# Performance work log

Hardware: AMD Instinct MI355X
Metric: run time of the kernel (lower is better)

The kernel has to match this reference:

```python
import jax, jax.numpy as jnp
import numpy as np

N = 100000
E = 1600000
DIM_IN, DIM_H, DIM_OUT = 48, 48, 48


def gcn_conv(x, edge_index, W, b):
    # PyG GCNConv: add self-loops, symmetric normalization D^-1/2 (A+I) D^-1/2, linear first.
    n = x.shape[0]
    loop = jnp.arange(n, dtype=edge_index.dtype)
    row = jnp.concatenate([edge_index[0], loop])  # sources
    col = jnp.concatenate([edge_index[1], loop])  # targets
    deg = jax.ops.segment_sum(jnp.ones_like(col, dtype=x.dtype), col, num_segments=n)
    dinv = jnp.where(deg > 0, jax.lax.rsqrt(jnp.maximum(deg, 1e-12)), 0.0)
    norm = dinv[row] * dinv[col]  # [E+N]
    h = x @ W  # [N, out]
    msg = h[row] * norm[:, None]  # gather + scale, [E+N, out]
    out = jax.ops.segment_sum(msg, col, num_segments=n)  # scatter-add
    return out + b


def setup_inputs() -> dict:
    key = jax.random.key(0)
    ks = jax.random.split(key, 8)
    x = jax.random.normal(ks[0], (N, DIM_IN), dtype=jnp.float32)
    edge_index = jax.random.randint(ks[1], (2, E), 0, N, dtype=jnp.int64)
    s1 = 1.0 / np.sqrt(DIM_IN)
    s2 = 1.0 / np.sqrt(DIM_H)
    s3 = 1.0 / np.sqrt(DIM_OUT)
    W1 = jax.random.uniform(ks[2], (DIM_IN, DIM_H), jnp.float32, -s1, s1)
    b1 = jnp.zeros((DIM_H,), jnp.float32)
    W2 = jax.random.uniform(ks[3], (DIM_H, DIM_OUT), jnp.float32, -s2, s2)
    b2 = jnp.zeros((DIM_OUT,), jnp.float32)
    Wlin = jax.random.uniform(ks[4], (DIM_OUT, 2), jnp.float32, -s3, s3)
    blin = jax.random.uniform(ks[5], (2,), jnp.float32, -s3, s3)
    return {"x": x, "edge_index": edge_index, "W1": W1, "b1": b1, "W2": W2, "b2": b2, "Wlin": Wlin, "blin": blin}


def reference(x, edge_index, W1, b1, W2, b2, Wlin, blin):
    h = gcn_conv(x, edge_index, W1, b1)
    h = jax.nn.leaky_relu(h, negative_slope=0.01)
    h = gcn_conv(h, edge_index, W2, b2)
    # global_add_pool with all-zero batch ids -> sum over all nodes, [1, DIM_OUT]
    g = jnp.sum(h, axis=0, keepdims=True)
    # dropout is identity in eval mode
    return g @ Wlin + blin  # [1, 2]
```

## Files before the change

kernel.cpp:

```cpp
#include <hip/hip_runtime.h>
#include <hip/hip_bf16.h>
#include <hip/hip_fp8.h>

#define DIM 48
#define HS8 64
#define BKN 128
#define CAP 2816
#define NB1MAX 800
#define NBLK 512
#define GNPB 64
#define GTPN 3

typedef float v2f __attribute__((ext_vector_type(2)));

__device__ inline unsigned pack_fp8x4(float a, float b, float c, float d) {
#if __has_builtin(__builtin_amdgcn_cvt_pk_fp8_f32)
    int w = __builtin_amdgcn_cvt_pk_fp8_f32(a, b, 0, false);
    w = __builtin_amdgcn_cvt_pk_fp8_f32(c, d, w, true);
    return (unsigned)w;
#else
    __hip_fp8_e4m3 qa(a), qb(b), qc(c), qd(d);
    return (unsigned)qa.__x | ((unsigned)qb.__x << 8) |
           ((unsigned)qc.__x << 16) | ((unsigned)qd.__x << 24);
#endif
}

__device__ inline void acc_fp8x4(unsigned w, float* acc) {
#if __has_builtin(__builtin_amdgcn_cvt_pk_f32_fp8)
    v2f lo = __builtin_amdgcn_cvt_pk_f32_fp8((int)w, false);
    v2f hi = __builtin_amdgcn_cvt_pk_f32_fp8((int)w, true);
    acc[0] += lo[0]; acc[1] += lo[1]; acc[2] += hi[0]; acc[3] += hi[1];
#else
    __hip_fp8_e4m3 q0, q1, q2, q3;
    q0.__x = (unsigned char)(w & 0xff);
    q1.__x = (unsigned char)((w >> 8) & 0xff);
    q2.__x = (unsigned char)((w >> 16) & 0xff);
    q3.__x = (unsigned char)(w >> 24);
    acc[0] += (float)q0; acc[1] += (float)q1;
    acc[2] += (float)q2; acc[3] += (float)q3;
#endif
}

__device__ inline void acc_fp8x16(uint4 v, float* acc) {
    acc_fp8x4(v.x, acc + 0);
    acc_fp8x4(v.y, acc + 4);
    acc_fp8x4(v.z, acc + 8);
    acc_fp8x4(v.w, acc + 12);
}

__global__ void k_zero(int* __restrict__ cntc, int* __restrict__ cntr,
                       float* __restrict__ g, int nb1) {
    int i = blockIdx.x * blockDim.x + threadIdx.x;
    if (i < nb1) { cntc[i] = 0; cntr[i] = 0; }
    if (i < 64) g[i] = 0.0f;
}

__global__ void k_part(const int* __restrict__ row, const int* __restrict__ col,
                       int* __restrict__ cntc, int* __restrict__ cntr,
                       unsigned* __restrict__ partc, unsigned* __restrict__ partr,
                       int E, int nb1) {
    __shared__ int hc[NB1MAX], hr[NB1MAX];
    __shared__ int bc_[NB1MAX], br_[NB1MAX];
    int blk = blockIdx.x, t = threadIdx.x;
    for (int i = t; i < nb1; i += blockDim.x) { hc[i] = 0; hr[i] = 0; }
    __syncthreads();
    int chunk = (E + NBLK - 1) / NBLK;
    int lo = blk * chunk, hi = min(lo + chunk, E);
    for (int e = lo + t; e < hi; e += blockDim.x) {
        atomicAdd(&hc[col[e] >> 7], 1);
        atomicAdd(&hr[row[e] >> 7], 1);
    }
    __syncthreads();
    for (int i = t; i < nb1; i += blockDim.x) {
        bc_[i] = hc[i] ? atomicAdd(&cntc[i], hc[i]) : 0;
        br_[i] = hr[i] ? atomicAdd(&cntr[i], hr[i]) : 0;
        hc[i] = 0; hr[i] = 0;
    }
    __syncthreads();
    for (int e = lo + t; e < hi; e += blockDim.x) {
        int c = col[e], r = row[e];
        int bc2 = c >> 7, br2 = r >> 7;
        unsigned pc = (unsigned)(bc_[bc2] + atomicAdd(&hc[bc2], 1));
        if (pc < (unsigned)CAP)
            partc[(size_t)bc2 * CAP + pc] = ((unsigned)(c & 127) << 24) | (unsigned)r;
        unsigned pr = (unsigned)(br_[br2] + atomicAdd(&hr[br2], 1));
        if (pr < (unsigned)CAP)
            partr[(size_t)br2 * CAP + pr] = ((unsigned)(r & 127) << 24) | (unsigned)c;
    }
}

__global__ void k_sortp(const unsigned* __restrict__ partc, const int* __restrict__ cntc,
                        int* __restrict__ nodpk, float* __restrict__ dinv,
                        int* __restrict__ srcs, int N, int nb1) {
    __shared__ int cnt[BKN];
    __shared__ int cur[BKN];
    __shared__ int sc[256];
    __shared__ int outb[CAP];
    int b = blockIdx.x, t = threadIdx.x;
    int nlo = b * BKN;
    int nE = min(cntc[b], CAP);
    const unsigned* pp = partc + (size_t)b * CAP;
    if (t < BKN) cnt[t] = 0;
    __syncthreads();
    for (int e = t; e < nE; e += blockDim.x)
        atomicAdd(&cnt[pp[e] >> 24], 1);
    __syncthreads();
    int v = (t < BKN) ? cnt[t] : 0;
    sc[t] = v;
    __syncthreads();
    for (int off = 1; off < 256; off <<= 1) {
        int u = (t >= off) ? sc[t - off] : 0;
        __syncthreads();
        sc[t] += u;
        __syncthreads();
    }
    int ex = (t == 0) ? 0 : sc[t - 1];
    if (t < BKN && nlo + t < N) {
        nodpk[nlo + t] = ex | (v << 16);
        dinv[nlo + t] = 1.0f / sqrtf((float)(v + 1));
        cur[t] = ex;
    }
    __syncthreads();
    for (int e = t; e < nE; e += blockDim.x) {
        unsigned p = pp[e];
        int s = atomicAdd(&cur[p >> 24], 1);
        outb[s] = (int)(p & 0xffffffu);
    }
    __syncthreads();
    int* sb = srcs + (size_t)b * CAP;
    for (int i2 = t; i2 < nE; i2 += blockDim.x) sb[i2] = outb[i2];
}

__global__ void k_wsum(const unsigned* __restrict__ partr, const int* __restrict__ cntr,
                       const float* __restrict__ dinv, float* __restrict__ wfin,
                       int N, int nb1) {
    __shared__ float ws[BKN];
    int b = blockIdx.x, t = threadIdx.x;
    if (t < BKN) ws[t] = 0.0f;
    __syncthreads();
    int nE = min(cntr[b], CAP);
    const unsigned* pp = partr + (size_t)b * CAP;
    for (int e = t; e < nE; e += blockDim.x) {
        unsigned p = pp[e];
        atomicAdd(&ws[p >> 24], dinv[p & 0xffffffu]);
    }
    __syncthreads();
    int j = b * BKN + t;
    if (t < BKN && j < N) {
        float dj = dinv[j];
        wfin[j] = (ws[t] + dj) * dj;
    }
}

__global__ void k_mm_scale(const float* __restrict__ in, const float* __restrict__ W,
                           const float* __restrict__ dinv,
                           unsigned char* __restrict__ hs8, int n) {
    __shared__ float Ws[DIM * DIM];
    for (int i = threadIdx.x; i < DIM * DIM; i += blockDim.x) Ws[i] = W[i];
    __syncthreads();
    int node = blockIdx.x * blockDim.x + threadIdx.x;
    if (node >= n) return;
    float xr[DIM];
    const float4* xp = (const float4*)(in + (size_t)node * DIM);
    #pragma unroll
    for (int j = 0; j < DIM / 4; ++j) {
        float4 v = xp[j];
        xr[j * 4 + 0] = v.x; xr[j * 4 + 1] = v.y;
        xr[j * 4 + 2] = v.z; xr[j * 4 + 3] = v.w;
    }
    float o[DIM];
    #pragma unroll
    for (int f = 0; f < DIM; ++f) o[f] = 0.0f;
    for (int k = 0; k < DIM; ++k) {
        float xv = xr[k];
        #pragma unroll
        for (int f = 0; f < DIM; ++f) o[f] = fmaf(xv, Ws[k * DIM + f], o[f]);
    }
    float d = dinv[node];
    uint4* hp = (uint4*)(hs8 + (size_t)node * HS8);
    #pragma unroll
    for (int q = 0; q < 3; ++q) {
        uint4 v;
        v.x = pack_fp8x4(o[q*16+ 0]*d, o[q*16+ 1]*d, o[q*16+ 2]*d, o[q*16+ 3]*d);
        v.y = pack_fp8x4(o[q*16+ 4]*d, o[q*16+ 5]*d, o[q*16+ 6]*d, o[q*16+ 7]*d);
        v.z = pack_fp8x4(o[q*16+ 8]*d, o[q*16+ 9]*d, o[q*16+10]*d, o[q*16+11]*d);
        v.w = pack_fp8x4(o[q*16+12]*d, o[q*16+13]*d, o[q*16+14]*d, o[q*16+15]*d);
        hp[q] = v;
    }
}

__global__ __launch_bounds__(GNPB * GTPN) void k_gather1f(
    const unsigned char* __restrict__ hs8,
    const int* __restrict__ nodpk, const int* __restrict__ srcs,
    const float* __restrict__ dinv, const float* __restrict__ wfin,
    const float* __restrict__ bias, float* __restrict__ g, int n) {
    __shared__ float gsum[DIM];
    int t = threadIdx.x;
    if (t < DIM) gsum[t] = 0.0f;
    __syncthreads();
    int local = t / GTPN;
    int c = t - local * GTPN;
    int i = blockIdx.x * GNPB + local;
    bool valid = (i < n);
    float ov[16];
    if (valid) {
        int pk = nodpk[i];
        int start = (i >> 7) * CAP + (pk & 0xffff);
        int end = start + (pk >> 16);
        float d = dinv[i];
        float w = wfin[i];
        const unsigned char* hb = hs8 + (size_t)c * 16;
        float acc[16];
        #pragma unroll
        for (int k = 0; k < 16; ++k) acc[k] = 0.0f;
        uint4 sv = *(const uint4*)(hb + (size_t)i * HS8);
        acc_fp8x16(sv, acc);
        for (int j = start; j < end; ++j) {
            uint4 v = *(const uint4*)(hb + (size_t)srcs[j] * HS8);
            acc_fp8x16(v, acc);
        }
        #pragma unroll
        for (int k = 0; k < 16; ++k) {
            float vv = acc[k] * d + bias[c * 16 + k];
            vv = (vv >= 0.0f) ? vv : 0.01f * vv;
            ov[k] = vv * w;
        }
    }
    if (valid) {
        #pragma unroll
        for (int k = 0; k < 16; ++k) atomicAdd(&gsum[c * 16 + k], ov[k]);
    }
    __syncthreads();
    if (t < DIM) atomicAdd(&g[t], gsum[t]);
}

__global__ void k_final2(const float* __restrict__ g, const float* __restrict__ W2,
                         const float* __restrict__ b2, const float* __restrict__ Wlin,
                         const float* __restrict__ blin, float* __restrict__ out, int n) {
    __shared__ float gp[DIM];
    int t = threadIdx.x;
    if (t < DIM) {
        float s = (float)n * b2[t];
        for (int q = 0; q < DIM; ++q) s += g[q] * W2[q * DIM + t];
        gp[t] = s;
    }
    __syncthreads();
    if (t < 2) {
        float s = blin[t];
        for (int f = 0; f < DIM; ++f) s += gp[f] * Wlin[f * 2 + t];
        out[t] = s;
    }
}

static inline char* alignup(char* p, size_t a) {
    return (char*)(((uintptr_t)p + a - 1) & ~(uintptr_t)(a - 1));
}

extern "C" void kernel_launch(void* const* d_in, const int* in_sizes, int n_in,
                              void* d_out, int out_size, void* d_ws, size_t ws_size,
                              hipStream_t stream) {
    const float* x    = (const float*)d_in[0];
    const int*   ei   = (const int*)d_in[1];
    const float* W1   = (const float*)d_in[2];
    const float* b1   = (const float*)d_in[3];
    const float* W2   = (const float*)d_in[4];
    const float* b2   = (const float*)d_in[5];
    const float* Wlin = (const float*)d_in[6];
    const float* blin = (const float*)d_in[7];
    float* out = (float*)d_out;

    int N = in_sizes[0] / DIM;
    int E = in_sizes[1] / 2;
    const int* row = ei;
    const int* col = ei + E;
    int nb1 = (N + BKN - 1) / BKN;

    char* p = (char*)d_ws;
    int* cntc = (int*)p;                  p = alignup(p + nb1 * 4, 64);
    int* cntr = (int*)p;                  p = alignup(p + nb1 * 4, 64);
    int* nodpk = (int*)p;                 p = alignup(p + (size_t)N * 4, 64);
    float* dinv = (float*)p;              p = alignup(p + (size_t)N * 4, 64);
    float* wfin = (float*)p;              p = alignup(p + (size_t)N * 4, 64);
    float* g = (float*)p;                 p = alignup(p + 64 * 4, 64);
    unsigned* partc = (unsigned*)p;       p = alignup(p + (size_t)nb1 * CAP * 4, 64);
    unsigned* partr = (unsigned*)p;       p = alignup(p + (size_t)nb1 * CAP * 4, 64);
    int* srcs = (int*)p;                  p = alignup(p + (size_t)nb1 * CAP * 4, 64);
    unsigned char* hs8 = (unsigned char*)p;

    int nblk = (N + 255) / 256;
    int gblk = (N + GNPB - 1) / GNPB;

    k_zero<<<(nb1 + 255) / 256, 256, 0, stream>>>(cntc, cntr, g, nb1);
    k_part<<<NBLK, 256, 0, stream>>>(row, col, cntc, cntr, partc, partr, E, nb1);
    k_sortp<<<nb1, 256, 0, stream>>>(partc, cntc, nodpk, dinv, srcs, N, nb1);
    k_wsum<<<nb1, 256, 0, stream>>>(partr, cntr, dinv, wfin, N, nb1);

    k_mm_scale<<<nblk, 256, 0, stream>>>(x, W1, dinv, hs8, N);
    k_gather1f<<<gblk, GNPB * GTPN, 0, stream>>>(hs8, nodpk, srcs, dinv, wfin, b1, g, N);

    k_final2<<<1, 64, 0, stream>>>(g, W2, b2, Wlin, blin, out, N);
}
```

Baseline: 174.5 us.

## Stage bucket partition in LDS for coalesced writes, split into two passes

The fused edge-partition kernel, which scattered each edge straight to global buckets, is replaced by a kernel that counts a chunk of edges into LDS, does a local prefix scan and sorts them into a shared staging buffer. Each wave then copies whole bucket runs to global memory contiguously. The column and row partitions now run as two separate launches with fewer, larger blocks. The aim is to turn scattered global writes into coalesced ones, at the cost of reading the edge arrays twice, a large LDS footprint that limits occupancy, and only 128 blocks per pass. The HS8 constant also changes from 64 to 48, which alters the hs8 row stride.

New measurement: 268.7 us. 54.0% more time.

```diff
diff --git a/kernel.cpp b/kernel.cpp
--- a/kernel.cpp
+++ b/kernel.cpp
@@ -3,11 +3,13 @@
 #include <hip/hip_fp8.h>
 
 #define DIM 48
-#define HS8 64
+#define HS8 48
 #define BKN 128
 #define CAP 2816
 #define NB1MAX 800
-#define NBLK 512
+#define NBLK2 128
+#define LCHUNK 12544
+#define NBPT 4
 #define GNPB 64
 #define GTPN 3
 
@@ -55,37 +57,67 @@
     if (i < 64) g[i] = 0.0f;
 }
 
-__global__ void k_part(const int* __restrict__ row, const int* __restrict__ col,
-                       int* __restrict__ cntc, int* __restrict__ cntr,
-                       unsigned* __restrict__ partc, unsigned* __restrict__ partr,
-                       int E, int nb1) {
-    __shared__ int hc[NB1MAX], hr[NB1MAX];
-    __shared__ int bc_[NB1MAX], br_[NB1MAX];
-    int blk = blockIdx.x, t = threadIdx.x;
-    for (int i = t; i < nb1; i += blockDim.x) { hc[i] = 0; hr[i] = 0; }
-    __syncthreads();
-    int chunk = (E + NBLK - 1) / NBLK;
-    int lo = blk * chunk, hi = min(lo + chunk, E);
-    for (int e = lo + t; e < hi; e += blockDim.x) {
-        atomicAdd(&hc[col[e] >> 7], 1);
-        atomicAdd(&hr[row[e] >> 7], 1);
-    }
-    __syncthreads();
-    for (int i = t; i < nb1; i += blockDim.x) {
-        bc_[i] = hc[i] ? atomicAdd(&cntc[i], hc[i]) : 0;
-        br_[i] = hr[i] ? atomicAdd(&cntr[i], hr[i]) : 0;
-        hc[i] = 0; hr[i] = 0;
-    }
-    __syncthreads();
-    for (int e = lo + t; e < hi; e += blockDim.x) {
-        int c = col[e], r = row[e];
-        int bc2 = c >> 7, br2 = r >> 7;
-        unsigned pc = (unsigned)(bc_[bc2] + atomicAdd(&hc[bc2], 1));
-        if (pc < (unsigned)CAP)
-            partc[(size_t)bc2 * CAP + pc] = ((unsigned)(c & 127) << 24) | (unsigned)r;
-        unsigned pr = (unsigned)(br_[br2] + atomicAdd(&hr[br2], 1));
-        if (pr < (unsigned)CAP)
-            partr[(size_t)br2 * CAP + pr] = ((unsigned)(r & 127) << 24) | (unsigned)c;
+__global__ __launch_bounds__(256) void k_part_wc(
+    const int* __restrict__ key, const int* __restrict__ pay,
+    int* __restrict__ cnt, unsigned* __restrict__ part, int E, int nb1) {
+    __shared__ int hist[NB1MAX];
+    __shared__ int lofs[NB1MAX];
+    __shared__ int lcur[NB1MAX];
+    __shared__ int sc[256];
+    __shared__ unsigned stage[LCHUNK];
+    int t = threadIdx.x;
+    int chunk = (E + NBLK2 - 1) / NBLK2;
+    int lo = blockIdx.x * chunk, hi = min(lo + chunk, E);
+    for (int tlo = lo; tlo < hi; tlo += LCHUNK) {
+        int thi = min(tlo + LCHUNK, hi);
+        for (int i = t; i < nb1; i += 256) hist[i] = 0;
+        __syncthreads();
+        for (int e = tlo + t; e < thi; e += 256)
+            atomicAdd(&hist[key[e] >> 7], 1);
+        __syncthreads();
+        int b0 = t * NBPT;
+        int s = 0;
+        #pragma unroll
+        for (int k = 0; k < NBPT; ++k) { int b = b0 + k; if (b < nb1) s += hist[b]; }
+        sc[t] = s;
+        __syncthreads();
+        for (int off = 1; off < 256; off <<= 1) {
+            int v = (t >= off) ? sc[t - off] : 0;
+            __syncthreads();
+            sc[t] += v;
+            __syncthreads();
+        }
+        int run = (t == 0) ? 0 : sc[t - 1];
+        #pragma unroll
+        for (int k = 0; k < NBPT; ++k) {
+            int b = b0 + k;
+            if (b < nb1) {
+                lofs[b] = run; lcur[b] = run;
+                int h = hist[b];
+                run += h;
+                hist[b] = h ? atomicAdd(&cnt[b], h) : 0;
+            }
+        }
+        __syncthreads();
+        for (int e = tlo + t; e < thi; e += 256) {
+            int ky = key[e];
+            int b = ky >> 7;
+            int sl = atomicAdd(&lcur[b], 1);
+            stage[sl] = ((unsigned)(ky & 127) << 24) | (unsigned)pay[e];
+        }
+        __syncthreads();
+        int wave = t >> 6, lane = t & 63;
+        for (int b = wave; b < nb1; b += 4) {
+            int lf = lofs[b];
+            int len = lcur[b] - lf;
+            int gb = hist[b];
+            unsigned* dst = part + (size_t)b * CAP;
+            for (int k = lane; k < len; k += 64) {
+                int d = gb + k;
+                if (d < CAP) dst[d] = stage[lf + k];
+            }
+        }
+        __syncthreads();
     }
 }
 
@@ -291,7 +323,8 @@
     int gblk = (N + GNPB - 1) / GNPB;
 
     k_zero<<<(nb1 + 255) / 256, 256, 0, stream>>>(cntc, cntr, g, nb1);
-    k_part<<<NBLK, 256, 0, stream>>>(row, col, cntc, cntr, partc, partr, E, nb1);
+    k_part_wc<<<NBLK2, 256, 0, stream>>>(col, row, cntc, partc, E, nb1);
+    k_part_wc<<<NBLK2, 256, 0, stream>>>(row, col, cntr, partr, E, nb1);
     k_sortp<<<nb1, 256, 0, stream>>>(partc, cntc, nodpk, dinv, srcs, N, nb1);
     k_wsum<<<nb1, 256, 0, stream>>>(partr, cntr, dinv, wfin, N, nb1);
 
```

## Use 256-node buckets, register-cached edge partitioning, and 48-byte fp8 rows

Applied to the files above, without the earlier changes.

Doubles the bucket size from 128 to 256 nodes, so there are half as many buckets and the block-local histograms and sort arrays map one node per thread. The partition kernel now loads each block's edges into registers once, instead of reading row and col from global memory in both the counting and the scatter passes. The fp8 feature row stride drops from 64 to 48 bytes, shrinking the gathered feature table so more of it stays in cache. The cost is larger per-bucket capacity buffers and more register use in the partition kernel, plus more LDS atomic contention per bucket.

Result: faster. 158.4 us (median of 2 runs) (-9.2%).

```diff
diff --git a/kernel.cpp b/kernel.cpp
--- a/kernel.cpp
+++ b/kernel.cpp
@@ -3,11 +3,12 @@
 #include <hip/hip_fp8.h>
 
 #define DIM 48
-#define HS8 64
-#define BKN 128
-#define CAP 2816
-#define NB1MAX 800
-#define NBLK 512
+#define HS8 48
+#define BKN 256
+#define BSH 8
+#define CAP 5248
+#define NB1MAX 400
+#define EPT 12
 #define GNPB 64
 #define GTPN 3
 
@@ -55,57 +56,62 @@
     if (i < 64) g[i] = 0.0f;
 }
 
-__global__ void k_part(const int* __restrict__ row, const int* __restrict__ col,
-                       int* __restrict__ cntc, int* __restrict__ cntr,
-                       unsigned* __restrict__ partc, unsigned* __restrict__ partr,
-                       int E, int nb1) {
+__global__ __launch_bounds__(256) void k_part(
+    const int* __restrict__ row, const int* __restrict__ col,
+    int* __restrict__ cntc, int* __restrict__ cntr,
+    unsigned* __restrict__ partc, unsigned* __restrict__ partr, int E, int nb1) {
     __shared__ int hc[NB1MAX], hr[NB1MAX];
     __shared__ int bc_[NB1MAX], br_[NB1MAX];
-    int blk = blockIdx.x, t = threadIdx.x;
-    for (int i = t; i < nb1; i += blockDim.x) { hc[i] = 0; hr[i] = 0; }
-    __syncthreads();
-    int chunk = (E + NBLK - 1) / NBLK;
-    int lo = blk * chunk, hi = min(lo + chunk, E);
-    for (int e = lo + t; e < hi; e += blockDim.x) {
-        atomicAdd(&hc[col[e] >> 7], 1);
-        atomicAdd(&hr[row[e] >> 7], 1);
-    }
-    __syncthreads();
-    for (int i = t; i < nb1; i += blockDim.x) {
+    int t = threadIdx.x;
+    int lo = blockIdx.x * (256 * EPT);
+    int hi = min(lo + 256 * EPT, E);
+    int ec[EPT], er[EPT];
+    int m = 0;
+    for (int e = lo + t; e < hi; e += 256) { ec[m] = col[e]; er[m] = row[e]; ++m; }
+    for (int i = t; i < nb1; i += 256) { hc[i] = 0; hr[i] = 0; }
+    __syncthreads();
+    for (int k = 0; k < m; ++k) {
+        atomicAdd(&hc[ec[k] >> BSH], 1);
+        atomicAdd(&hr[er[k] >> BSH], 1);
+    }
+    __syncthreads();
+    for (int i = t; i < nb1; i += 256) {
         bc_[i] = hc[i] ? atomicAdd(&cntc[i], hc[i]) : 0;
         br_[i] = hr[i] ? atomicAdd(&cntr[i], hr[i]) : 0;
         hc[i] = 0; hr[i] = 0;
     }
     __syncthreads();
-    for (int e = lo + t; e < hi; e += blockDim.x) {
-        int c = col[e], r = row[e];
-        int bc2 = c >> 7, br2 = r >> 7;
-        unsigned pc = (unsigned)(bc_[bc2] + atomicAdd(&hc[bc2], 1));
-        if (pc < (unsigned)CAP)
-            partc[(size_t)bc2 * CAP + pc] = ((unsigned)(c & 127) << 24) | (unsigned)r;
-        unsigned pr = (unsigned)(br_[br2] + atomicAdd(&hr[br2], 1));
-        if (pr < (unsigned)CAP)
-            partr[(size_t)br2 * CAP + pr] = ((unsigned)(r & 127) << 24) | (unsigned)c;
-    }
-}
-
-__global__ void k_sortp(const unsigned* __restrict__ partc, const int* __restrict__ cntc,
-                        int* __restrict__ nodpk, float* __restrict__ dinv,
-                        int* __restrict__ srcs, int N, int nb1) {
+    for (int k = 0; k < m; ++k) {
+        int c = ec[k], r = er[k];
+        int b1 = c >> BSH;
+        unsigned p1 = (unsigned)(bc_[b1] + atomicAdd(&hc[b1], 1));
+        if (p1 < (unsigned)CAP)
+            partc[(size_t)b1 * CAP + p1] = ((unsigned)(c & (BKN - 1)) << 24) | (unsigned)r;
+        int b2 = r >> BSH;
+        unsigned p2 = (unsigned)(br_[b2] + atomicAdd(&hr[b2], 1));
+        if (p2 < (unsigned)CAP)
+            partr[(size_t)b2 * CAP + p2] = ((unsigned)(r & (BKN - 1)) << 24) | (unsigned)c;
+    }
+}
+
+__global__ __launch_bounds__(256) void k_sortp(
+    const unsigned* __restrict__ partc, const int* __restrict__ cntc,
+    int* __restrict__ nodpk, float* __restrict__ dinv,
+    int* __restrict__ srcs, int N, int nb1) {
     __shared__ int cnt[BKN];
     __shared__ int cur[BKN];
     __shared__ int sc[256];
     __shared__ int outb[CAP];
     int b = blockIdx.x, t = threadIdx.x;
-    int nlo = b * BKN;
+    int nlo = b << BSH;
     int nE = min(cntc[b], CAP);
     const unsigned* pp = partc + (size_t)b * CAP;
-    if (t < BKN) cnt[t] = 0;
-    __syncthreads();
-    for (int e = t; e < nE; e += blockDim.x)
+    cnt[t] = 0;
+    __syncthreads();
+    for (int e = t; e < nE; e += 256)
         atomicAdd(&cnt[pp[e] >> 24], 1);
     __syncthreads();
-    int v = (t < BKN) ? cnt[t] : 0;
+    int v = cnt[t];
     sc[t] = v;
     __syncthreads();
     for (int off = 1; off < 256; off <<= 1) {
@@ -115,38 +121,38 @@
         __syncthreads();
     }
     int ex = (t == 0) ? 0 : sc[t - 1];
-    if (t < BKN && nlo + t < N) {
+    if (nlo + t < N) {
         nodpk[nlo + t] = ex | (v << 16);
         dinv[nlo + t] = 1.0f / sqrtf((float)(v + 1));
-        cur[t] = ex;
-    }
-    __syncthreads();
-    for (int e = t; e < nE; e += blockDim.x) {
+    }
+    cur[t] = ex;
+    __syncthreads();
+    for (int e = t; e < nE; e += 256) {
         unsigned p = pp[e];
         int s = atomicAdd(&cur[p >> 24], 1);
         outb[s] = (int)(p & 0xffffffu);
     }
     __syncthreads();
     int* sb = srcs + (size_t)b * CAP;
-    for (int i2 = t; i2 < nE; i2 += blockDim.x) sb[i2] = outb[i2];
-}
-
-__global__ void k_wsum(const unsigned* __restrict__ partr, const int* __restrict__ cntr,
-                       const float* __restrict__ dinv, float* __restrict__ wfin,
-                       int N, int nb1) {
+    for (int i2 = t; i2 < nE; i2 += 256) sb[i2] = outb[i2];
+}
+
+__global__ __launch_bounds__(256) void k_wsum(
+    const unsigned* __restrict__ partr, const int* __restrict__ cntr,
+    const float* __restrict__ dinv, float* __restrict__ wfin, int N, int nb1) {
     __shared__ float ws[BKN];
     int b = blockIdx.x, t = threadIdx.x;
-    if (t < BKN) ws[t] = 0.0f;
+    ws[t] = 0.0f;
     __syncthreads();
     int nE = min(cntr[b], CAP);
     const unsigned* pp = partr + (size_t)b * CAP;
-    for (int e = t; e < nE; e += blockDim.x) {
+    for (int e = t; e < nE; e += 256) {
         unsigned p = pp[e];
         atomicAdd(&ws[p >> 24], dinv[p & 0xffffffu]);
     }
     __syncthreads();
-    int j = b * BKN + t;
-    if (t < BKN && j < N) {
+    int j = (b << BSH) + t;
+    if (j < N) {
         float dj = dinv[j];
         wfin[j] = (ws[t] + dj) * dj;
     }
@@ -205,7 +211,7 @@
     float ov[16];
     if (valid) {
         int pk = nodpk[i];
-        int start = (i >> 7) * CAP + (pk & 0xffff);
+        int start = (i >> BSH) * CAP + (pk & 0xffff);
         int end = start + (pk >> 16);
         float d = dinv[i];
         float w = wfin[i];
@@ -289,9 +295,10 @@
 
     int nblk = (N + 255) / 256;
     int gblk = (N + GNPB - 1) / GNPB;
+    int pblk = (E + 256 * EPT - 1) / (256 * EPT);
 
     k_zero<<<(nb1 + 255) / 256, 256, 0, stream>>>(cntc, cntr, g, nb1);
-    k_part<<<NBLK, 256, 0, stream>>>(row, col, cntc, cntr, partc, partr, E, nb1);
+    k_part<<<pblk, 256, 0, stream>>>(row, col, cntc, cntr, partc, partr, E, nb1);
     k_sortp<<<nb1, 256, 0, stream>>>(partc, cntc, nodpk, dinv, srcs, N, nb1);
     k_wsum<<<nb1, 256, 0, stream>>>(partr, cntr, dinv, wfin, N, nb1);
 
```
